# Kernel tuning notes

Measured on AMD Instinct MI355X. Metric: run time of the kernel, lower is better.

Reference implementation:

```python
import jax, jax.numpy as jnp
import numpy as np

B, T, I, H, C = 8192, 28, 28, 128, 10


def setup_inputs() -> dict:
    key = jax.random.key(0)
    ks = jax.random.split(key, 7)
    s_ih = 1.0 / np.sqrt(H)
    return {
        "x": jax.random.normal(ks[0], (B, T, I), dtype=jnp.float32),
        "W_ih": jax.random.normal(ks[1], (4 * H, I), dtype=jnp.float32) * s_ih,
        "W_hh": jax.random.normal(ks[2], (4 * H, H), dtype=jnp.float32) * s_ih,
        "b_ih": jax.random.normal(ks[3], (4 * H,), dtype=jnp.float32) * s_ih,
        "b_hh": jax.random.normal(ks[4], (4 * H,), dtype=jnp.float32) * s_ih,
        "W_fc": jax.random.normal(ks[5], (C, H), dtype=jnp.float32) * s_ih,
        "b_fc": jnp.zeros((C,), dtype=jnp.float32),
    }


def reference(x, W_ih, W_hh, b_ih, b_hh, W_fc, b_fc):
    # x: [B, T, I]. PyTorch LSTM gate order: i, f, g, o.
    b = b_ih + b_hh  # [4H]
    # Precompute input projections for all timesteps: [T, B, 4H]
    x_proj = jnp.einsum("bti,gi->tbg", x, W_ih) + b
    h0 = jnp.zeros((x.shape[0], H), dtype=x.dtype)
    c0 = jnp.zeros_like(h0)

    def step(carry, xp_t):
        h, c = carry
        gates = xp_t + h @ W_hh.T  # [B, 4H]
        i_g, f_g, g_g, o_g = jnp.split(gates, 4, axis=-1)
        i_g = jax.nn.sigmoid(i_g)
        f_g = jax.nn.sigmoid(f_g)
        g_g = jnp.tanh(g_g)
        o_g = jax.nn.sigmoid(o_g)
        c = f_g * c + i_g * g_g
        h = o_g * jnp.tanh(c)
        return (h, c), None

    (h_last, _), _ = jax.lax.scan(step, (h0, c0), x_proj)
    # outputs[:, -1, :] == final hidden state; fc + relu
    return jax.nn.relu(h_last @ W_fc.T + b_fc)
```

## Files before the change

### kernel.cpp

```cpp
#include <hip/hip_runtime.h>
#include <math.h>

typedef __attribute__((ext_vector_type(8))) _Float16 half8;
typedef __attribute__((ext_vector_type(4))) _Float16 half4;
typedef __attribute__((ext_vector_type(4))) float    f32x4;
typedef __attribute__((ext_vector_type(2))) float    f32x2;

#define TSTEPS 28
#define IDIM   28
#define HDIM   128
#define NKC    5
#define TILE_B 32
#define CDIM   10

#if __has_builtin(__builtin_amdgcn_exp2f)
#define EXP2F(x) __builtin_amdgcn_exp2f(x)
#else
#define EXP2F(x) exp2f(x)
#endif
#if __has_builtin(__builtin_amdgcn_rcpf)
#define RCPF(x) __builtin_amdgcn_rcpf(x)
#else
#define RCPF(x) (1.0f / (x))
#endif

#define NLOG2E (-1.44269504f)
#define P2LOG2E (2.88539008f)

#define MFMA16(a,b,c) __builtin_amdgcn_mfma_f32_16x16x32_f16((a),(b),(c),0,0,0)

__global__ __launch_bounds__(256) void pack_w(const float* __restrict__ Wih,
                                              const float* __restrict__ Whh,
                                              const float* __restrict__ bih,
                                              const float* __restrict__ bhh,
                                              _Float16* __restrict__ P) {
    int e = blockIdx.x * 256 + threadIdx.x;
    if (e >= NKC * 4 * 8 * 64 * 8) return;
    int j  = e & 7;
    int ln = (e >> 3) & 63;
    int w  = (e >> 9) & 7;
    int t  = (e >> 12) & 3;
    int kc = e >> 14;
    int k  = kc * 32 + ((ln >> 4) << 3) + j;
    int u  = w * 16 + (ln & 15);
    int g  = t * HDIM + u;
    float v = 0.f;
    if (k < HDIM)                   v = Whh[g * HDIM + k];
    else if (k < HDIM + IDIM)       v = Wih[g * IDIM + (k - HDIM)];
    else if (k == HDIM + IDIM)      v = bih[g] + bhh[g];
    float sc = (t == 2) ? P2LOG2E : NLOG2E;
    P[e] = (_Float16)(v * sc);
}

__global__ __launch_bounds__(1024, 4) void lstm_kernel(
    const float* __restrict__ x,
    const _Float16* __restrict__ P,
    const float* __restrict__ Wfc,
    const float* __restrict__ b_fc,
    float* __restrict__ out)
{
    __shared__ __align__(16) _Float16 frag[2][4][64][8];
    __shared__ __align__(16) _Float16 Plds[4][8][64][8];
    __shared__ __align__(16) float hplain[TILE_B][HDIM + 4];

    const int tid = threadIdx.x;
    const int l   = tid & 63;
    const int w   = tid >> 6;
    const int sid = w >> 3;
    const int w8  = w & 7;
    const int b0  = blockIdx.x * TILE_B;

    {
        const float4* P4 = (const float4*)P;
        float4* dst = (float4*)Plds;
        dst[tid]        = P4[8192 + tid];
        dst[tid + 1024] = P4[9216 + tid];
    }
    half8 breg[4][4];
    {
        const half8* Pp = (const half8*)P;
        #pragma unroll
        for (int kc = 0; kc < 4; ++kc)
            #pragma unroll
            for (int g = 0; g < 4; ++g)
                breg[g][kc] = Pp[((kc * 4 + g) * 8 + w8) * 64 + l];
    }

    {
        float4 z = {0.f, 0.f, 0.f, 0.f};
        if (tid < 512) ((float4*)frag)[tid] = z;
    }

    const int l15 = l & 15;
    const int u    = w8 * 16 + l15;
    const int kc_h = w8 >> 1;
    const int quad = (2 * w8 + ((l >> 3) & 1)) & 3;
    const int jh   = l & 7;
    const int mb   = (l >> 4) << 2;
    _Float16 (*myfrag)[64][8] = frag[sid];

    const float* xp = x + (size_t)(b0 + sid * 16 + l15) * (TSTEPS * IDIM)
                        + 8 * (l >> 4);
    const int o2 = (l < 48) ? 4 : 0;

    f32x4 acc[4];
    f32x2 cst01 = {0.f, 0.f}, cst23 = {0.f, 0.f};
    const f32x4 zc = {0.f, 0.f, 0.f, 0.f};
    half8 a4;
    float4 xv0, xv1;

    auto cvt_a4 = [&](float4 v0, float4 v1) {
        if (l >= 48) v1 = (float4){1.f, 0.f, 0.f, 0.f};
        half8 r;
        r[0] = (_Float16)v0.x; r[1] = (_Float16)v0.y;
        r[2] = (_Float16)v0.z; r[3] = (_Float16)v0.w;
        r[4] = (_Float16)v1.x; r[5] = (_Float16)v1.y;
        r[6] = (_Float16)v1.z; r[7] = (_Float16)v1.w;
        a4 = r;
    };

    cvt_a4(*(const float4*)(xp), *(const float4*)(xp + o2));

    auto mfma_phase = [&](int t) {
        if (t + 1 < TSTEPS) {
            xv0 = *(const float4*)(xp + (t + 1) * IDIM);
            xv1 = *(const float4*)(xp + (t + 1) * IDIM + o2);
        }
        half8 A0 = *(const half8*)&myfrag[0][l][0];
        half8 A1 = *(const half8*)&myfrag[1][l][0];
        half8 A2 = *(const half8*)&myfrag[2][l][0];
        half8 A3 = *(const half8*)&myfrag[3][l][0];
        #pragma unroll
        for (int g = 0; g < 4; ++g) {
            half8 pb = *(const half8*)&Plds[g][w8][l][0];
            acc[g] = MFMA16(a4, pb, zc);
        }
        #pragma unroll
        for (int g = 0; g < 4; ++g) acc[g] = MFMA16(A0, breg[g][0], acc[g]);
        #pragma unroll
        for (int g = 0; g < 4; ++g) acc[g] = MFMA16(A1, breg[g][1], acc[g]);
        #pragma unroll
        for (int g = 0; g < 4; ++g) acc[g] = MFMA16(A2, breg[g][2], acc[g]);
        #pragma unroll
        for (int g = 0; g < 4; ++g) acc[g] = MFMA16(A3, breg[g][3], acc[g]);
    };

    auto act_phase = [&](int t) {
        const bool lastT = (t == TSTEPS - 1);
        float hv[4];
        #pragma unroll
        for (int rp = 0; rp < 2; ++rp) {
            const int r0 = rp * 2, r1 = r0 + 1;
            f32x2 Ei = {EXP2F(acc[0][r0]), EXP2F(acc[0][r1])};
            f32x2 Ef = {EXP2F(acc[1][r0]), EXP2F(acc[1][r1])};
            f32x2 Eg = {EXP2F(acc[2][r0]), EXP2F(acc[2][r1])};
            f32x2 Eo = {EXP2F(acc[3][r0]), EXP2F(acc[3][r1])};
            f32x2 one = {1.f, 1.f};
            f32x2 Di = Ei + one, Df = Ef + one, Dg = Eg + one, Do = Eo + one;
            f32x2 Pif = Di * Df, Pgo = Dg * Do;
            f32x2 Rif = {RCPF(Pif.x), RCPF(Pif.y)};
            f32x2 Rgo = {RCPF(Pgo.x), RCPF(Pgo.y)};
            f32x2 is = Rif * Df, fs = Rif * Di;
            f32x2 gt = one - 2.f * (Rgo * Do);
            f32x2 os = Rgo * Dg;
            f32x2 cstp = rp ? cst23 : cst01;
            f32x2 c = fs * cstp + is * gt;
            if (rp) cst23 = c; else cst01 = c;
            f32x2 Etc = {EXP2F(c.x * P2LOG2E), EXP2F(c.y * P2LOG2E)};
            f32x2 Dtc = Etc + one;
            f32x2 Rtc = {RCPF(Dtc.x), RCPF(Dtc.y)};
            f32x2 tc = one - 2.f * Rtc;
            f32x2 h2 = os * tc;
            hv[r0] = h2.x; hv[r1] = h2.y;
        }
        if (lastT) {
            #pragma unroll
            for (int r = 0; r < 4; ++r)
                hplain[sid * 16 + mb + r][u] = hv[r];
        } else {
            #pragma unroll
            for (int r = 0; r < 4; ++r)
                myfrag[kc_h][mb + r + 16 * quad][jh] = (_Float16)hv[r];
            cvt_a4(xv0, xv1);
        }
    };

    __syncthreads();

    if (sid == 0) mfma_phase(0);
    __syncthreads();

    for (int t = 0; t < TSTEPS; ++t) {
        if (sid == 0) act_phase(t);
        else          mfma_phase(t);
        __syncthreads();
        if (sid == 0) { if (t + 1 < TSTEPS) mfma_phase(t + 1); }
        else          act_phase(t);
        __syncthreads();
    }

    if (tid < TILE_B * CDIM) {
        int row = tid / CDIM, c = tid % CDIM;
        const float4* hv4 = (const float4*)&hplain[row][0];
        const float4* wf  = (const float4*)(Wfc + c * HDIM);
        float s = b_fc[c];
        #pragma unroll
        for (int q = 0; q < 32; ++q) {
            float4 a4v = hv4[q], b4 = wf[q];
            s += a4v.x * b4.x + a4v.y * b4.y + a4v.z * b4.z + a4v.w * b4.w;
        }
        out[(size_t)(b0 + row) * CDIM + c] = fmaxf(s, 0.f);
    }
}

extern "C" void kernel_launch(void* const* d_in, const int* in_sizes, int n_in,
                              void* d_out, int out_size, void* d_ws, size_t ws_size,
                              hipStream_t stream) {
    const float* x   = (const float*)d_in[0];
    const float* Wih = (const float*)d_in[1];
    const float* Whh = (const float*)d_in[2];
    const float* bih = (const float*)d_in[3];
    const float* bhh = (const float*)d_in[4];
    const float* Wfc = (const float*)d_in[5];
    const float* bfc = (const float*)d_in[6];
    float* out = (float*)d_out;
    _Float16* P = (_Float16*)d_ws;

    hipLaunchKernelGGL(pack_w, dim3(320), dim3(256), 0, stream, Wih, Whh, bih, bhh, P);
    hipLaunchKernelGGL(lstm_kernel, dim3(8192 / TILE_B), dim3(1024), 0, stream,
                       x, P, Wfc, bfc, out);
}
```

Before: 133.4 us.

## Replace ping-pong group schedule with double-buffered fused per-step loop, one barrier

Drops the staggered schedule where the two 8-wave groups alternated MFMA and activation phases across two barriers per timestep. Each wave now does MFMA and activation in the same iteration, writing h into a double-buffered fragment so only one barrier per step is needed. Plds and hplain now share one LDS buffer, since hplain is only written after the recurrence. The cost is losing the overlap of one group's MFMA with the other group's transcendental math, and the ubuf alias depends on every wave finishing its Plds reads before the hplain writes.

```diff
diff --git a/kernel.cpp b/kernel.cpp
--- a/kernel.cpp
+++ b/kernel.cpp
@@ -59,20 +59,21 @@
     const float* __restrict__ b_fc,
     float* __restrict__ out)
 {
-    __shared__ __align__(16) _Float16 frag[2][4][64][8];
-    __shared__ __align__(16) _Float16 Plds[4][8][64][8];
-    __shared__ __align__(16) float hplain[TILE_B][HDIM + 4];
+    __shared__ __align__(16) _Float16 frag[2][2][4][64][8];
+    __shared__ __align__(16) char ubuf[4 * 8 * 64 * 8 * 2];
+    _Float16 (*Plds)[8][64][8] = (_Float16 (*)[8][64][8])ubuf;
+    float (*hplain)[HDIM + 4]  = (float (*)[HDIM + 4])ubuf;
 
     const int tid = threadIdx.x;
     const int l   = tid & 63;
     const int w   = tid >> 6;
-    const int sid = w >> 3;
+    const int grp = w >> 3;
     const int w8  = w & 7;
     const int b0  = blockIdx.x * TILE_B;
 
     {
         const float4* P4 = (const float4*)P;
-        float4* dst = (float4*)Plds;
+        float4* dst = (float4*)ubuf;
         dst[tid]        = P4[8192 + tid];
         dst[tid + 1024] = P4[9216 + tid];
     }
@@ -97,17 +98,15 @@
     const int quad = (2 * w8 + ((l >> 3) & 1)) & 3;
     const int jh   = l & 7;
     const int mb   = (l >> 4) << 2;
-    _Float16 (*myfrag)[64][8] = frag[sid];
-
-    const float* xp = x + (size_t)(b0 + sid * 16 + l15) * (TSTEPS * IDIM)
+
+    const float* xp = x + (size_t)(b0 + grp * 16 + l15) * (TSTEPS * IDIM)
                         + 8 * (l >> 4);
     const int o2 = (l < 48) ? 4 : 0;
 
-    f32x4 acc[4];
     f32x2 cst01 = {0.f, 0.f}, cst23 = {0.f, 0.f};
     const f32x4 zc = {0.f, 0.f, 0.f, 0.f};
     half8 a4;
-    float4 xv0, xv1;
+    float hv[4];
 
     auto cvt_a4 = [&](float4 v0, float4 v1) {
         if (l >= 48) v1 = (float4){1.f, 0.f, 0.f, 0.f};
@@ -121,15 +120,18 @@
 
     cvt_a4(*(const float4*)(xp), *(const float4*)(xp + o2));
 
-    auto mfma_phase = [&](int t) {
-        if (t + 1 < TSTEPS) {
-            xv0 = *(const float4*)(xp + (t + 1) * IDIM);
-            xv1 = *(const float4*)(xp + (t + 1) * IDIM + o2);
-        }
-        half8 A0 = *(const half8*)&myfrag[0][l][0];
-        half8 A1 = *(const half8*)&myfrag[1][l][0];
-        half8 A2 = *(const half8*)&myfrag[2][l][0];
-        half8 A3 = *(const half8*)&myfrag[3][l][0];
+    __syncthreads();
+
+    for (int t = 0; t < TSTEPS; ++t) {
+        const _Float16 (*cur)[64][8] = frag[t & 1][grp];
+        _Float16 (*nxt)[64][8]       = frag[(t + 1) & 1][grp];
+        const bool more = (t + 1 < TSTEPS);
+
+        half8 A0 = *(const half8*)&cur[0][l][0];
+        half8 A1 = *(const half8*)&cur[1][l][0];
+        half8 A2 = *(const half8*)&cur[2][l][0];
+        half8 A3 = *(const half8*)&cur[3][l][0];
+        f32x4 acc[4];
         #pragma unroll
         for (int g = 0; g < 4; ++g) {
             half8 pb = *(const half8*)&Plds[g][w8][l][0];
@@ -143,11 +145,13 @@
         for (int g = 0; g < 4; ++g) acc[g] = MFMA16(A2, breg[g][2], acc[g]);
         #pragma unroll
         for (int g = 0; g < 4; ++g) acc[g] = MFMA16(A3, breg[g][3], acc[g]);
-    };
-
-    auto act_phase = [&](int t) {
-        const bool lastT = (t == TSTEPS - 1);
-        float hv[4];
+
+        float4 xv0, xv1;
+        if (more) {
+            xv0 = *(const float4*)(xp + (t + 1) * IDIM);
+            xv1 = *(const float4*)(xp + (t + 1) * IDIM + o2);
+        }
+
         #pragma unroll
         for (int rp = 0; rp < 2; ++rp) {
             const int r0 = rp * 2, r1 = r0 + 1;
@@ -173,31 +177,20 @@
             f32x2 h2 = os * tc;
             hv[r0] = h2.x; hv[r1] = h2.y;
         }
-        if (lastT) {
+
+        if (more) {
             #pragma unroll
             for (int r = 0; r < 4; ++r)
-                hplain[sid * 16 + mb + r][u] = hv[r];
-        } else {
-            #pragma unroll
-            for (int r = 0; r < 4; ++r)
-                myfrag[kc_h][mb + r + 16 * quad][jh] = (_Float16)hv[r];
+                nxt[kc_h][mb + r + 16 * quad][jh] = (_Float16)hv[r];
             cvt_a4(xv0, xv1);
         }
-    };
-
+        __syncthreads();
+    }
+
+    #pragma unroll
+    for (int r = 0; r < 4; ++r)
+        hplain[grp * 16 + mb + r][u] = hv[r];
     __syncthreads();
-
-    if (sid == 0) mfma_phase(0);
-    __syncthreads();
-
-    for (int t = 0; t < TSTEPS; ++t) {
-        if (sid == 0) act_phase(t);
-        else          mfma_phase(t);
-        __syncthreads();
-        if (sid == 0) { if (t + 1 < TSTEPS) mfma_phase(t + 1); }
-        else          act_phase(t);
-        __syncthreads();
-    }
 
     if (tid < TILE_B * CDIM) {
         int row = tid / CDIM, c = tid % CDIM;
```

Result: faster. 124.5 us (-6.7%).
